# Performance work log

Measured on AMD Instinct MI355X. Metric: run time of the kernel, lower is better.

Reference implementation:

```python
import jax, jax.numpy as jnp
import numpy as np

NUM_HEADS = 16
NUM_KV_HEADS = 4
ROPE_BASE = 10000.0
TRAIN_SEQ_LEN = 2048


def _rms_norm(x):
    eps = jnp.asarray(jnp.finfo(x.dtype).eps, x.dtype)
    return x * jax.lax.rsqrt(jnp.mean(x * x, axis=-1, keepdims=True) + eps)


def _rope_cos_sin(seq_len, head_dim, dtype):
    # seq_len <= TRAIN_SEQ_LEN -> no NTK rescaling, matches Rotary buffer path
    half = head_dim // 2
    inv_freq = 1.0 / (ROPE_BASE ** (jnp.arange(0, head_dim, 2, dtype=jnp.float32) / head_dim))
    t = jnp.arange(seq_len, dtype=jnp.float32)
    freqs = jnp.outer(t, inv_freq)  # [S, half]
    cos = jnp.cos(freqs)[None, :, None, :].astype(dtype)
    sin = jnp.sin(freqs)[None, :, None, :].astype(dtype)
    return cos, sin


def _apply_rotary(x, cos, sin):
    half = x.shape[-1] // 2
    x1, x2 = x[..., :half], x[..., half:]
    return jnp.concatenate([x1 * cos + x2 * sin, -x1 * sin + x2 * cos], axis=-1)


def setup_inputs() -> dict:
    key = jax.random.key(0)
    ks = jax.random.split(key, 5)
    B, S, D = 2, 2048, 2048
    kv_dim = NUM_KV_HEADS * (D // NUM_HEADS)
    sw = 0.02
    return {
        "x": jax.random.normal(ks[0], (B, S, D), jnp.float32),
        "Wq": jax.random.normal(ks[1], (D, D), jnp.float32) * sw,
        "Wk": jax.random.normal(ks[2], (kv_dim, D), jnp.float32) * sw,
        "Wv": jax.random.normal(ks[3], (kv_dim, D), jnp.float32) * sw,
        "Wproj": jax.random.normal(ks[4], (D, D), jnp.float32) * sw,
        "q_gain": jnp.ones((NUM_HEADS,), jnp.float32),
    }


def reference(x, Wq, Wk, Wv, Wproj, q_gain):
    B, S, D = x.shape
    H, Hkv = NUM_HEADS, NUM_KV_HEADS
    hd = D // H
    r = H // Hkv

    q = (x @ Wq.T).reshape(B, S, H, hd)
    k = (x @ Wk.T).reshape(B, S, Hkv, hd)
    v = (x @ Wv.T).reshape(B, S, Hkv, hd)

    q = _rms_norm(q)
    k = _rms_norm(k)

    cos, sin = _rope_cos_sin(S, hd, q.dtype)
    q = _apply_rotary(q, cos, sin)
    k = _apply_rotary(k, cos, sin)
    q = q * q_gain.astype(q.dtype)[None, None, :, None]

    # GQA: repeat kv heads (repeat_interleave along head dim)
    k = jnp.repeat(k, r, axis=2)  # [B,S,H,hd]
    v = jnp.repeat(v, r, axis=2)

    scale = 1.0 / jnp.sqrt(jnp.asarray(hd, q.dtype))
    scores = jnp.einsum("bqhd,bkhd->bhqk", q, k) * scale
    causal = jnp.tril(jnp.ones((S, S), dtype=bool))
    scores = jnp.where(causal[None, None], scores, jnp.asarray(-jnp.inf, scores.dtype))
    attn = jax.nn.softmax(scores, axis=-1)
    y = jnp.einsum("bhqk,bkhd->bqhd", attn, v)

    return y.reshape(B, S, D) @ Wproj.T
```

## Files before the change

kernel.cpp:

```cpp
#include <hip/hip_runtime.h>

#define D_MODEL 2048
#define SEQ 2048
#define BATCH 2
#define NH 16
#define NKV 4
#define HD 128
#define KVD (NKV * HD)
#define QKVN (D_MODEL + 2 * KVD)
#define MROWS (BATCH * SEQ)

typedef __attribute__((ext_vector_type(8))) short short8;
typedef __attribute__((ext_vector_type(4))) float f32x4;

__device__ __forceinline__ unsigned short f2bf(float f) {
    union { float f; unsigned int u; } v; v.f = f;
    unsigned int r = (v.u + 0x7FFFu + ((v.u >> 16) & 1u)) >> 16;
    return (unsigned short)r;
}

__device__ __forceinline__ unsigned short f2bf_pos(float f) {
    union { float f; unsigned int u; } v; v.f = f;
    return (unsigned short)((v.u + 0x8000u) >> 16);
}

__device__ __forceinline__ float bf2f(unsigned short u) {
    union { float f; unsigned int i; } v; v.i = ((unsigned int)u) << 16;
    return v.f;
}

__device__ __forceinline__ void async16(const void* g, void* l) {
    __builtin_amdgcn_global_load_lds((const __attribute__((address_space(1))) void*)g,
                                     (__attribute__((address_space(3))) void*)l, 16, 0, 0);
}

__global__ __launch_bounds__(256) void cast_all(const float* __restrict__ x,
                                                const float* __restrict__ wq,
                                                const float* __restrict__ wk,
                                                const float* __restrict__ wv,
                                                const float* __restrict__ wp,
                                                unsigned short* __restrict__ xb,
                                                unsigned short* __restrict__ wqkv,
                                                unsigned short* __restrict__ wpb) {
    int i = blockIdx.x * 256 + threadIdx.x;
    const float4* s; ushort4* d; int j;
    if (i < 2097152)      { s = (const float4*)x;  d = (ushort4*)xb;             j = i; }
    else if (i < 3145728) { s = (const float4*)wq; d = (ushort4*)wqkv;           j = i - 2097152; }
    else if (i < 3407872) { s = (const float4*)wk; d = (ushort4*)wqkv + 1048576; j = i - 3145728; }
    else if (i < 3670016) { s = (const float4*)wv; d = (ushort4*)wqkv + 1310720; j = i - 3407872; }
    else                  { s = (const float4*)wp; d = (ushort4*)wpb;            j = i - 3670016; }
    float4 v = s[j];
    ushort4 o;
    o.x = f2bf(v.x); o.y = f2bf(v.y); o.z = f2bf(v.z); o.w = f2bf(v.w);
    d[j] = o;
}

__global__ __launch_bounds__(256) void gemm_qkv(const unsigned short* __restrict__ A,
                                                const unsigned short* __restrict__ W,
                                                const float* __restrict__ gain,
                                                unsigned short* __restrict__ qbuf,
                                                unsigned short* __restrict__ kbuf,
                                                unsigned short* __restrict__ vtb) {
    __shared__ unsigned short smem[128 * 137];
    unsigned short* tile = smem;
    const int K = D_MODEL;
    const int tid  = threadIdx.x;
    const int lane = tid & 63;
    const int wave = tid >> 6;
    const int qm   = lane & 15;
    const int quad = lane >> 4;
    const int m0 = blockIdx.y * 128;
    const int bx = blockIdx.x;
    const int n0 = bx * 128;
    const int wm = (wave >> 1) * 64;
    const int wn = (wave & 1) * 64;

    f32x4 acc[4][4];
#pragma unroll
    for (int i = 0; i < 4; i++)
#pragma unroll
        for (int j = 0; j < 4; j++) acc[i][j] = (f32x4){0.f, 0.f, 0.f, 0.f};

    const int r1 = tid >> 2;
    const int c1 = (((tid & 3) ^ ((tid >> 3) & 3)) * 8);
    const unsigned short* Ag = A + (size_t)(m0 + r1) * K + c1;
    const unsigned short* Wg = W + (size_t)(n0 + r1) * K + c1;
    const int stg = wave * 512;
    const int swq = ((qm >> 1) & 3) * 8;

#define STG_Q(bufv) \
    async16(Ag,                  &smem[(bufv) * 4096 + stg]); \
    async16(Ag + (size_t)64 * K, &smem[(bufv) * 4096 + 2048 + stg]); \
    async16(Wg,                  &smem[8192 + (bufv) * 4096 + stg]); \
    async16(Wg + (size_t)64 * K, &smem[8192 + (bufv) * 4096 + 2048 + stg]); \
    Ag += 32; Wg += 32;

#define CMP_Q(bufv) { \
    short8 af[4], bfr[4]; \
    _Pragma("unroll") \
    for (int i = 0; i < 4; i++) { \
        af[i]  = *(const short8*)&smem[(bufv) * 4096 + (wm + i * 16 + qm) * 32 + (quad * 8 ^ swq)]; \
        bfr[i] = *(const short8*)&smem[8192 + (bufv) * 4096 + (wn + i * 16 + qm) * 32 + (quad * 8 ^ swq)]; \
    } \
    __builtin_amdgcn_s_setprio(1); \
    _Pragma("unroll") \
    for (int mi = 0; mi < 4; mi++) \
        _Pragma("unroll") \
        for (int ni = 0; ni < 4; ni++) \
            acc[mi][ni] = __builtin_amdgcn_mfma_f32_16x16x32_bf16(af[mi], bfr[ni], acc[mi][ni], 0, 0, 0); \
    __builtin_amdgcn_s_setprio(0); \
}

    STG_Q(0)
    for (int t = 0; t < 31; ++t) {
        STG_Q(1)
        asm volatile("s_waitcnt vmcnt(4)\n\ts_barrier" ::: "memory");
        CMP_Q(0)
        asm volatile("s_barrier" ::: "memory");
        STG_Q(0)
        asm volatile("s_waitcnt vmcnt(4)\n\ts_barrier" ::: "memory");
        CMP_Q(1)
        asm volatile("s_barrier" ::: "memory");
    }
    STG_Q(1)
    asm volatile("s_waitcnt vmcnt(4)\n\ts_barrier" ::: "memory");
    CMP_Q(0)
    asm volatile("s_waitcnt vmcnt(0)\n\ts_barrier" ::: "memory");
    CMP_Q(1)
    __syncthreads();
#undef STG_Q
#undef CMP_Q

#pragma unroll
    for (int mi = 0; mi < 4; mi++)
#pragma unroll
        for (int r = 0; r < 4; r++) {
            int row = wm + mi * 16 + quad * 4 + r;
#pragma unroll
            for (int ni = 0; ni < 4; ni++)
                tile[row * 137 + wn + ni * 16 + qm] = f2bf(acc[mi][ni][r]);
        }
    __syncthreads();

    const int s_base = m0 & 2047;
    const int bb = m0 >> 11;
    if (bx < 20) {
        const bool isq = bx < 16;
        const float g = isq ? gain[bx] * 0.12751744f : 1.0f;
        unsigned short* dst = isq
            ? qbuf + ((size_t)(bb * NH + bx) * SEQ + s_base) * HD
            : kbuf + ((size_t)(bb * NKV + (bx - 16)) * SEQ + s_base) * HD;
        const float invf = __builtin_amdgcn_exp2f(-(float)lane * 0.20761871f - 2.6514961f);
        for (int rr = 0; rr < 32; rr++) {
            int row = wave * 32 + rr;
            float x1 = bf2f(tile[row * 137 + lane]);
            float x2 = bf2f(tile[row * 137 + 64 + lane]);
            float ss = x1 * x1 + x2 * x2;
            ss += __shfl_xor(ss, 1);  ss += __shfl_xor(ss, 2);  ss += __shfl_xor(ss, 4);
            ss += __shfl_xor(ss, 8);  ss += __shfl_xor(ss, 16); ss += __shfl_xor(ss, 32);
            float rs = rsqrtf(ss * (1.0f / 128.0f) + 1.1920929e-07f);
            float rev = (float)(s_base + row) * invf;
            rev -= truncf(rev);
            float sn = __builtin_amdgcn_sinf(rev);
            float cs = __builtin_amdgcn_cosf(rev);
            float a1 = x1 * rs, a2 = x2 * rs;
            float o1 = (a1 * cs + a2 * sn) * g;
            float o2 = (a2 * cs - a1 * sn) * g;
            dst[(size_t)row * HD + lane]      = f2bf(o1);
            dst[(size_t)row * HD + 64 + lane] = f2bf(o2);
        }
    } else {
        const int hk = bx - 20;
        unsigned short* dst = vtb + ((size_t)(bb * NKV + hk) * HD) * SEQ + s_base;
        const int sc = (tid & 31) * 4;
        const int d0 = tid >> 5;
#pragma unroll
        for (int i = 0; i < 16; i++) {
            int d = d0 + 8 * i;
            ushort4 ov;
            ov.x = tile[(sc + 0) * 137 + d];
            ov.y = tile[(sc + 1) * 137 + d];
            ov.z = tile[(sc + 2) * 137 + d];
            ov.w = tile[(sc + 3) * 137 + d];
            *(ushort4*)(dst + (size_t)d * SEQ + sc) = ov;
        }
    }
}

__global__ __launch_bounds__(256) void gemm_bt(const unsigned short* __restrict__ A,
                                               const unsigned short* __restrict__ W,
                                               float* __restrict__ C, int M, int N, int K) {
    __shared__ unsigned short smem[16384];
    const int tid  = threadIdx.x;
    const int lane = tid & 63;
    const int wave = tid >> 6;
    const int qm   = lane & 15;
    const int quad = lane >> 4;
    const int m0 = blockIdx.y * 128;
    const int n0 = blockIdx.x * 128;
    const int wm = (wave >> 1) * 64;
    const int wn = (wave & 1) * 64;

    f32x4 acc[4][4];
#pragma unroll
    for (int i = 0; i < 4; i++)
#pragma unroll
        for (int j = 0; j < 4; j++) acc[i][j] = (f32x4){0.f, 0.f, 0.f, 0.f};

    const int r1 = tid >> 2;
    const int c1 = (((tid & 3) ^ ((tid >> 3) & 3)) * 8);
    const unsigned short* Ag = A + (size_t)(m0 + r1) * K + c1;
    const unsigned short* Wg = W + (size_t)(n0 + r1) * K + c1;
    const int stg = wave * 512;
    const int swq = ((qm >> 1) & 3) * 8;

#define STG_B(bufv) \
    async16(Ag,                  &smem[(bufv) * 4096 + stg]); \
    async16(Ag + (size_t)64 * K, &smem[(bufv) * 4096 + 2048 + stg]); \
    async16(Wg,                  &smem[8192 + (bufv) * 4096 + stg]); \
    async16(Wg + (size_t)64 * K, &smem[8192 + (bufv) * 4096 + 2048 + stg]); \
    Ag += 32; Wg += 32;

#define CMP_B(bufv) { \
    short8 af[4], bfr[4]; \
    _Pragma("unroll") \
    for (int i = 0; i < 4; i++) { \
        af[i]  = *(const short8*)&smem[(bufv) * 4096 + (wm + i * 16 + qm) * 32 + (quad * 8 ^ swq)]; \
        bfr[i] = *(const short8*)&smem[8192 + (bufv) * 4096 + (wn + i * 16 + qm) * 32 + (quad * 8 ^ swq)]; \
    } \
    __builtin_amdgcn_s_setprio(1); \
    _Pragma("unroll") \
    for (int mi = 0; mi < 4; mi++) \
        _Pragma("unroll") \
        for (int ni = 0; ni < 4; ni++) \
            acc[mi][ni] = __builtin_amdgcn_mfma_f32_16x16x32_bf16(af[mi], bfr[ni], acc[mi][ni], 0, 0, 0); \
    __builtin_amdgcn_s_setprio(0); \
}

    STG_B(0)
    for (int t = 0; t < 31; ++t) {
        STG_B(1)
        asm volatile("s_waitcnt vmcnt(4)\n\ts_barrier" ::: "memory");
        CMP_B(0)
        asm volatile("s_barrier" ::: "memory");
        STG_B(0)
        asm volatile("s_waitcnt vmcnt(4)\n\ts_barrier" ::: "memory");
        CMP_B(1)
        asm volatile("s_barrier" ::: "memory");
    }
    STG_B(1)
    asm volatile("s_waitcnt vmcnt(4)\n\ts_barrier" ::: "memory");
    CMP_B(0)
    asm volatile("s_waitcnt vmcnt(0)\n\ts_barrier" ::: "memory");
    CMP_B(1)
#undef STG_B
#undef CMP_B

#pragma unroll
    for (int mi = 0; mi < 4; mi++) {
#pragma unroll
        for (int r = 0; r < 4; r++) {
            int row = m0 + wm + mi * 16 + quad * 4 + r;
            float* Crow = C + (size_t)row * N + n0 + wn + qm;
#pragma unroll
            for (int ni = 0; ni < 4; ni++) Crow[ni * 16] = acc[mi][ni][r];
        }
    }
}

__global__ __launch_bounds__(256, 4) void attn(const unsigned short* __restrict__ qb,
                                               const unsigned short* __restrict__ kb,
                                               const unsigned short* __restrict__ vt,
                                               const float* __restrict__ gain,
                                               unsigned short* __restrict__ y) {
    __shared__ unsigned short Ks[8192];
    __shared__ unsigned short Vs[8192];
    __shared__ unsigned short plds[4][1024];
    const int tid  = threadIdx.x;
    const int lane = tid & 63;
    const int wave = tid >> 6;
    const int bh   = blockIdx.x & 31;
    const int g4   = blockIdx.x >> 5;
    const int gg = g4 & 7;
    const int gs = g4 >> 3;
    const int qt64 = (gs == 0) ? gg : (gs == 1) ? (31 - gg) : (gs == 2) ? (8 + gg) : (23 - gg);
    const int h = bh & 15;
    const int b = bh >> 4;
    const int qm   = lane & 15;
    const int quad = lane >> 4;
    const int q0    = qt64 * 64;
    const int qrow0 = q0 + wave * 16;
    const float M = 17.0f * fabsf(gain[h]);

    const unsigned short* Qp = qb + (((size_t)(b * NH + h)) * SEQ + qrow0) * HD;
    const unsigned short* Kp = kb + ((size_t)(b * NKV + (h >> 2))) * SEQ * HD;
    const unsigned short* Vp = vt + ((size_t)(b * NKV + (h >> 2))) * HD * SEQ;

    short8 qf[4];
#pragma unroll
    for (int c = 0; c < 4; c++)
        qf[c] = *(const short8*)(Qp + qm * HD + c * 32 + quad * 8);

    f32x4 o[8];
#pragma unroll
    for (int t = 0; t < 8; t++) o[t] = (f32x4){0.f, 0.f, 0.f, 0.f};
    float lr[4] = {0.f, 0.f, 0.f, 0.f};

    const unsigned short* KsA = Kp + (size_t)(tid >> 4) * HD + (((tid & 15) ^ (tid >> 4)) & 15) * 8;
    const unsigned short* VsA = Vp + (size_t)(tid >> 3) * SEQ + (((tid & 7) ^ ((tid >> 3) & 7)) * 8);
    char* KsB = (char*)Ks + wave * 1024;
    char* VsB = (char*)Vs + wave * 1024;
    unsigned short* P = &plds[wave][0];

    const int kvend = q0 + 64;
    for (int kv0 = 0; kv0 < kvend; kv0 += 64) {
#pragma unroll
        for (int i = 0; i < 4; i++) {
            async16(KsA + (size_t)(16 * i) * HD,  KsB + i * 4096);
            async16(VsA + (size_t)(32 * i) * SEQ, VsB + i * 4096);
        }
        KsA += (size_t)64 * HD;
        VsA += 64;
        __syncthreads();

        f32x4 s[4];
#pragma unroll
        for (int g = 0; g < 4; g++) s[g] = (f32x4){0.f, 0.f, 0.f, 0.f};
#pragma unroll
        for (int c = 0; c < 4; c++) {
#pragma unroll
            for (int g = 0; g < 4; g++) {
                short8 kf = *(const short8*)&Ks[(g * 16 + qm) * 128 + (((c * 4 + quad) ^ qm) * 8)];
                s[g] = __builtin_amdgcn_mfma_f32_16x16x32_bf16(qf[c], kf, s[g], 0, 0, 0);
            }
        }
        if (kv0 + 63 > qrow0) {
#pragma unroll
            for (int g = 0; g < 4; g++)
#pragma unroll
                for (int r = 0; r < 4; r++) {
                    int qg = qrow0 + quad * 4 + r;
                    if (kv0 + g * 16 + qm > qg) s[g][r] = -3.0e38f;
                }
        }
        float p[4][4];
#pragma unroll
        for (int g = 0; g < 4; g++)
#pragma unroll
            for (int r = 0; r < 4; r++) {
                p[g][r] = __builtin_amdgcn_exp2f(s[g][r] - M);
                lr[r] += p[g][r];
            }
#pragma unroll
        for (int g = 0; g < 4; g++)
#pragma unroll
            for (int r = 0; r < 4; r++) {
                int rowp = quad * 4 + r;
                P[rowp * 64 + (((g * 2 + (qm >> 3)) ^ (rowp & 7)) * 8) + (qm & 7)] = f2bf_pos(p[g][r]);
            }
        short8 pa[2];
#pragma unroll
        for (int ka = 0; ka < 2; ka++)
            pa[ka] = *(const short8*)&P[qm * 64 + (((ka * 4 + quad) ^ (qm & 7)) * 8)];
#pragma unroll
        for (int t = 0; t < 8; t++) {
#pragma unroll
            for (int ka = 0; ka < 2; ka++) {
                short8 vf = *(const short8*)&Vs[(t * 16 + qm) * 64 + (((ka * 4 + quad) ^ (qm & 7)) * 8)];
                o[t] = __builtin_amdgcn_mfma_f32_16x16x32_bf16(pa[ka], vf, o[t], 0, 0, 0);
            }
        }
        __syncthreads();
    }
    float rl[4];
#pragma unroll
    for (int r = 0; r < 4; r++) {
        float l = lr[r];
        l += __shfl_xor(l, 1);
        l += __shfl_xor(l, 2);
        l += __shfl_xor(l, 4);
        l += __shfl_xor(l, 8);
        rl[r] = 1.0f / l;
    }
#pragma unroll
    for (int t = 0; t < 8; t++) {
#pragma unroll
        for (int r = 0; r < 4; r++) {
            size_t row = (size_t)(b * SEQ + qrow0 + quad * 4 + r);
            y[row * D_MODEL + h * HD + t * 16 + qm] = f2bf(o[t][r] * rl[r]);
        }
    }
}

extern "C" void kernel_launch(void* const* d_in, const int* in_sizes, int n_in,
                              void* d_out, int out_size, void* d_ws, size_t ws_size,
                              hipStream_t stream) {
    const float* x  = (const float*)d_in[0];
    const float* Wq = (const float*)d_in[1];
    const float* Wk = (const float*)d_in[2];
    const float* Wv = (const float*)d_in[3];
    const float* Wp = (const float*)d_in[4];
    const float* qg = (const float*)d_in[5];

    char* ws = (char*)d_ws;
    unsigned short* xb   = (unsigned short*)(ws + 0);
    unsigned short* wqkv = (unsigned short*)(ws + 16777216);
    unsigned short* wp   = (unsigned short*)(ws + 29360128);
    unsigned short* qbuf = (unsigned short*)(ws + 37748736);
    unsigned short* kbuf = (unsigned short*)(ws + 54525952);
    unsigned short* vtb  = (unsigned short*)(ws + 58720256);
    unsigned short* y    = xb;

    cast_all<<<18432, 256, 0, stream>>>(x, Wq, Wk, Wv, Wp, xb, wqkv, wp);
    gemm_qkv<<<dim3(24, 32), 256, 0, stream>>>(xb, wqkv, qg, qbuf, kbuf, vtb);
    attn<<<1024, 256, 0, stream>>>(qbuf, kbuf, vtb, qg, y);
    gemm_bt<<<dim3(16, 32), 256, 0, stream>>>(y, wp, (float*)d_out, MROWS, D_MODEL, D_MODEL);
}
```

Baseline: 292.2 us.

## Enlarge QKV GEMM to 256x256 tiles with 8 waves and ping-pong pipeline

The fused QKV projection GEMM moves from 128x128 tiles with 4 waves to 256x256 tiles with 8 waves and 512 threads per block. Each K step is now 64 wide and staged in quarter-tile pieces that interleave with MFMA groups, with double-buffered LDS. The epilogue (RMSNorm, RoPE and the V transpose) is done in two halves that reuse the LDS. The intent is more operand reuse per byte loaded and better overlap of loads with MFMA, at the cost of a much smaller grid (192 blocks on a chip with more CUs) and 128KB of LDS per block, which limits occupancy.

```diff
diff --git a/kernel.cpp b/kernel.cpp
--- a/kernel.cpp
+++ b/kernel.cpp
@@ -55,13 +55,13 @@
     d[j] = o;
 }
 
-__global__ __launch_bounds__(256) void gemm_qkv(const unsigned short* __restrict__ A,
+__global__ __launch_bounds__(512) void gemm_qkv(const unsigned short* __restrict__ A,
                                                 const unsigned short* __restrict__ W,
                                                 const float* __restrict__ gain,
                                                 unsigned short* __restrict__ qbuf,
                                                 unsigned short* __restrict__ kbuf,
                                                 unsigned short* __restrict__ vtb) {
-    __shared__ unsigned short smem[128 * 137];
+    __shared__ unsigned short smem[65536];
     unsigned short* tile = smem;
     const int K = D_MODEL;
     const int tid  = threadIdx.x;
@@ -69,120 +69,169 @@
     const int wave = tid >> 6;
     const int qm   = lane & 15;
     const int quad = lane >> 4;
-    const int m0 = blockIdx.y * 128;
+    const int wr   = wave >> 2;
+    const int wc   = wave & 3;
+    const int m0 = blockIdx.y * 256;
     const int bx = blockIdx.x;
-    const int n0 = bx * 128;
-    const int wm = (wave >> 1) * 64;
-    const int wn = (wave & 1) * 64;
-
-    f32x4 acc[4][4];
-#pragma unroll
-    for (int i = 0; i < 4; i++)
-#pragma unroll
-        for (int j = 0; j < 4; j++) acc[i][j] = (f32x4){0.f, 0.f, 0.f, 0.f};
-
-    const int r1 = tid >> 2;
-    const int c1 = (((tid & 3) ^ ((tid >> 3) & 3)) * 8);
-    const unsigned short* Ag = A + (size_t)(m0 + r1) * K + c1;
-    const unsigned short* Wg = W + (size_t)(n0 + r1) * K + c1;
-    const int stg = wave * 512;
-    const int swq = ((qm >> 1) & 3) * 8;
-
-#define STG_Q(bufv) \
-    async16(Ag,                  &smem[(bufv) * 4096 + stg]); \
-    async16(Ag + (size_t)64 * K, &smem[(bufv) * 4096 + 2048 + stg]); \
-    async16(Wg,                  &smem[8192 + (bufv) * 4096 + stg]); \
-    async16(Wg + (size_t)64 * K, &smem[8192 + (bufv) * 4096 + 2048 + stg]); \
-    Ag += 32; Wg += 32;
-
-#define CMP_Q(bufv) { \
-    short8 af[4], bfr[4]; \
+    const int n0 = bx * 256;
+
+    f32x4 acc[2][2][4][2];
+#pragma unroll
+    for (int a = 0; a < 2; a++)
+#pragma unroll
+        for (int b = 0; b < 2; b++)
+#pragma unroll
+            for (int c = 0; c < 4; c++)
+#pragma unroll
+                for (int d = 0; d < 2; d++) acc[a][b][c][d] = (f32x4){0.f, 0.f, 0.f, 0.f};
+
+    const unsigned short* Asrc = A + (size_t)(m0 + (tid >> 3)) * K + (((tid & 7) ^ ((tid >> 3) & 7)) * 8);
+    const unsigned short* Bsrc = W + (size_t)(n0 + (tid >> 3)) * K + (((tid & 7) ^ ((tid >> 3) & 7)) * 8);
+    const int dstg = tid * 8;
+    const int ck0 = ((quad ^ (qm & 7)) * 8);
+    const int ck1 = (((4 + quad) ^ (qm & 7)) * 8);
+    const int arow = wr * 64 + qm;
+    const int brow = wc * 32 + qm;
+
+    short8 af[4][2], bf0[2][2], bf1[2][2];
+
+#define STG_A(mh, bufv, kt1) \
+    async16(Asrc + (size_t)((mh) * 128) * K + (kt1),      &smem[(bufv) * 16384 + (mh) * 8192 + dstg]); \
+    async16(Asrc + (size_t)((mh) * 128 + 64) * K + (kt1), &smem[(bufv) * 16384 + (mh) * 8192 + 4096 + dstg]);
+#define STG_B(nh, bufv, kt1) \
+    async16(Bsrc + (size_t)((nh) * 128) * K + (kt1),      &smem[32768 + (bufv) * 16384 + (nh) * 8192 + dstg]); \
+    async16(Bsrc + (size_t)((nh) * 128 + 64) * K + (kt1), &smem[32768 + (bufv) * 16384 + (nh) * 8192 + 4096 + dstg]);
+
+#define RD_A(ab, mh) { \
     _Pragma("unroll") \
-    for (int i = 0; i < 4; i++) { \
-        af[i]  = *(const short8*)&smem[(bufv) * 4096 + (wm + i * 16 + qm) * 32 + (quad * 8 ^ swq)]; \
-        bfr[i] = *(const short8*)&smem[8192 + (bufv) * 4096 + (wn + i * 16 + qm) * 32 + (quad * 8 ^ swq)]; \
-    } \
+    for (int m = 0; m < 4; m++) { \
+        af[m][0] = *(const short8*)&smem[(ab) + ((mh) * 128 + arow + m * 16) * 64 + ck0]; \
+        af[m][1] = *(const short8*)&smem[(ab) + ((mh) * 128 + arow + m * 16) * 64 + ck1]; \
+    } }
+#define RD_B(bb, nh, dstf) { \
+    _Pragma("unroll") \
+    for (int n = 0; n < 2; n++) { \
+        dstf[n][0] = *(const short8*)&smem[(bb) + ((nh) * 128 + brow + n * 16) * 64 + ck0]; \
+        dstf[n][1] = *(const short8*)&smem[(bb) + ((nh) * 128 + brow + n * 16) * 64 + ck1]; \
+    } }
+#define MFMA16(mh, nh, bfr) { \
     __builtin_amdgcn_s_setprio(1); \
     _Pragma("unroll") \
-    for (int mi = 0; mi < 4; mi++) \
+    for (int m = 0; m < 4; m++) \
         _Pragma("unroll") \
-        for (int ni = 0; ni < 4; ni++) \
-            acc[mi][ni] = __builtin_amdgcn_mfma_f32_16x16x32_bf16(af[mi], bfr[ni], acc[mi][ni], 0, 0, 0); \
-    __builtin_amdgcn_s_setprio(0); \
-}
-
-    STG_Q(0)
-    for (int t = 0; t < 31; ++t) {
-        STG_Q(1)
-        asm volatile("s_waitcnt vmcnt(4)\n\ts_barrier" ::: "memory");
-        CMP_Q(0)
-        asm volatile("s_barrier" ::: "memory");
-        STG_Q(0)
-        asm volatile("s_waitcnt vmcnt(4)\n\ts_barrier" ::: "memory");
-        CMP_Q(1)
-        asm volatile("s_barrier" ::: "memory");
-    }
-    STG_Q(1)
-    asm volatile("s_waitcnt vmcnt(4)\n\ts_barrier" ::: "memory");
-    CMP_Q(0)
-    asm volatile("s_waitcnt vmcnt(0)\n\ts_barrier" ::: "memory");
-    CMP_Q(1)
-    __syncthreads();
-#undef STG_Q
-#undef CMP_Q
-
-#pragma unroll
-    for (int mi = 0; mi < 4; mi++)
-#pragma unroll
-        for (int r = 0; r < 4; r++) {
-            int row = wm + mi * 16 + quad * 4 + r;
-#pragma unroll
-            for (int ni = 0; ni < 4; ni++)
-                tile[row * 137 + wn + ni * 16 + qm] = f2bf(acc[mi][ni][r]);
-        }
-    __syncthreads();
+        for (int n = 0; n < 2; n++) { \
+            acc[mh][nh][m][n] = __builtin_amdgcn_mfma_f32_16x16x32_bf16(af[m][0], bfr[n][0], acc[mh][nh][m][n], 0, 0, 0); \
+            acc[mh][nh][m][n] = __builtin_amdgcn_mfma_f32_16x16x32_bf16(af[m][1], bfr[n][1], acc[mh][nh][m][n], 0, 0, 0); \
+        } \
+    __builtin_amdgcn_s_setprio(0); }
+
+#define BARv asm volatile("s_barrier" ::: "memory")
+#define WV4  asm volatile("s_waitcnt vmcnt(4)" ::: "memory")
+#define WV2  asm volatile("s_waitcnt vmcnt(2)" ::: "memory")
+#define WV0  asm volatile("s_waitcnt vmcnt(0)" ::: "memory")
+
+#define STEP(p, kt1) { \
+     RD_A((p)*16384, 0) RD_B(32768 + (p)*16384, 0, bf0) STG_A(0, (p)^1, kt1) \
+    BARv; MFMA16(0, 0, bf0) WV4; BARv; \
+     RD_B(32768 + (p)*16384, 1, bf1) STG_B(0, (p)^1, kt1) \
+    BARv; MFMA16(0, 1, bf1) WV4; BARv; \
+     RD_A((p)*16384, 1) STG_B(1, (p)^1, kt1) \
+    BARv; MFMA16(1, 0, bf0) BARv; \
+     STG_A(1, (p)^1, kt1) \
+    BARv; MFMA16(1, 1, bf1) WV4; BARv; \
+}
+#define STEPE(p) { \
+    RD_A((p)*16384, 0) RD_B(32768 + (p)*16384, 0, bf0) BARv; MFMA16(0, 0, bf0) WV2; BARv; \
+    RD_B(32768 + (p)*16384, 1, bf1)                    BARv; MFMA16(0, 1, bf1) WV0; BARv; \
+    RD_A((p)*16384, 1)                                 BARv; MFMA16(1, 0, bf0) BARv; \
+    MFMA16(1, 1, bf1) \
+}
+
+    STG_A(0, 0, 0) STG_B(0, 0, 0) STG_B(1, 0, 0) STG_A(1, 0, 0)
+    WV4; BARv;
+
+#pragma unroll 1
+    for (int t2 = 0; t2 < 15; ++t2) {
+        STEP(0, t2 * 128 + 64)
+        STEP(1, t2 * 128 + 128)
+    }
+    STEP(0, 1984)
+    STEPE(1)
+#undef STG_A
+#undef STG_B
+#undef RD_A
+#undef RD_B
+#undef MFMA16
+#undef STEP
+#undef STEPE
 
     const int s_base = m0 & 2047;
     const int bb = m0 >> 11;
-    if (bx < 20) {
-        const bool isq = bx < 16;
-        const float g = isq ? gain[bx] * 0.12751744f : 1.0f;
-        unsigned short* dst = isq
-            ? qbuf + ((size_t)(bb * NH + bx) * SEQ + s_base) * HD
-            : kbuf + ((size_t)(bb * NKV + (bx - 16)) * SEQ + s_base) * HD;
-        const float invf = __builtin_amdgcn_exp2f(-(float)lane * 0.20761871f - 2.6514961f);
-        for (int rr = 0; rr < 32; rr++) {
-            int row = wave * 32 + rr;
-            float x1 = bf2f(tile[row * 137 + lane]);
-            float x2 = bf2f(tile[row * 137 + 64 + lane]);
-            float ss = x1 * x1 + x2 * x2;
-            ss += __shfl_xor(ss, 1);  ss += __shfl_xor(ss, 2);  ss += __shfl_xor(ss, 4);
-            ss += __shfl_xor(ss, 8);  ss += __shfl_xor(ss, 16); ss += __shfl_xor(ss, 32);
-            float rs = rsqrtf(ss * (1.0f / 128.0f) + 1.1920929e-07f);
-            float rev = (float)(s_base + row) * invf;
-            rev -= truncf(rev);
-            float sn = __builtin_amdgcn_sinf(rev);
-            float cs = __builtin_amdgcn_cosf(rev);
-            float a1 = x1 * rs, a2 = x2 * rs;
-            float o1 = (a1 * cs + a2 * sn) * g;
-            float o2 = (a2 * cs - a1 * sn) * g;
-            dst[(size_t)row * HD + lane]      = f2bf(o1);
-            dst[(size_t)row * HD + 64 + lane] = f2bf(o2);
-        }
-    } else {
-        const int hk = bx - 20;
-        unsigned short* dst = vtb + ((size_t)(bb * NKV + hk) * HD) * SEQ + s_base;
-        const int sc = (tid & 31) * 4;
-        const int d0 = tid >> 5;
-#pragma unroll
-        for (int i = 0; i < 16; i++) {
-            int d = d0 + 8 * i;
-            ushort4 ov;
-            ov.x = tile[(sc + 0) * 137 + d];
-            ov.y = tile[(sc + 1) * 137 + d];
-            ov.z = tile[(sc + 2) * 137 + d];
-            ov.w = tile[(sc + 3) * 137 + d];
-            *(ushort4*)(dst + (size_t)d * SEQ + sc) = ov;
+    const float invf = __builtin_amdgcn_exp2f(-(float)lane * 0.20761871f - 2.6514961f);
+
+#pragma unroll
+    for (int half = 0; half < 2; ++half) {
+        __syncthreads();
+#pragma unroll
+        for (int nh = 0; nh < 2; nh++)
+#pragma unroll
+            for (int m = 0; m < 4; m++)
+#pragma unroll
+                for (int n = 0; n < 2; n++)
+#pragma unroll
+                    for (int r = 0; r < 4; r++) {
+                        int row = wr * 64 + m * 16 + quad * 4 + r;
+                        int col = nh * 128 + wc * 32 + n * 16 + qm;
+                        tile[row * 264 + col] = f2bf(acc[half][nh][m][n][r]);
+                    }
+        __syncthreads();
+
+        if (bx < 10) {
+            const bool isq = bx < 8;
+#pragma unroll
+            for (int hh = 0; hh < 2; hh++) {
+                const int h = (isq ? 2 * bx : (bx - 8) * 2) + hh;
+                const float g = isq ? gain[h] * 0.12751744f : 1.0f;
+                unsigned short* dst = isq
+                    ? qbuf + ((size_t)(bb * NH + h) * SEQ + s_base + half * 128) * HD
+                    : kbuf + ((size_t)(bb * NKV + h) * SEQ + s_base + half * 128) * HD;
+                for (int rr = 0; rr < 16; rr++) {
+                    int row = wave * 16 + rr;
+                    float x1 = bf2f(tile[row * 264 + hh * 128 + lane]);
+                    float x2 = bf2f(tile[row * 264 + hh * 128 + 64 + lane]);
+                    float ss = x1 * x1 + x2 * x2;
+                    ss += __shfl_xor(ss, 1);  ss += __shfl_xor(ss, 2);  ss += __shfl_xor(ss, 4);
+                    ss += __shfl_xor(ss, 8);  ss += __shfl_xor(ss, 16); ss += __shfl_xor(ss, 32);
+                    float rs = rsqrtf(ss * (1.0f / 128.0f) + 1.1920929e-07f);
+                    float rev = (float)(s_base + half * 128 + row) * invf;
+                    rev -= truncf(rev);
+                    float sn = __builtin_amdgcn_sinf(rev);
+                    float cs = __builtin_amdgcn_cosf(rev);
+                    float a1 = x1 * rs, a2 = x2 * rs;
+                    float o1 = (a1 * cs + a2 * sn) * g;
+                    float o2 = (a2 * cs - a1 * sn) * g;
+                    dst[(size_t)row * HD + lane]      = f2bf(o1);
+                    dst[(size_t)row * HD + 64 + lane] = f2bf(o2);
+                }
+            }
+        } else {
+            const int sc = (tid & 31) * 4;
+            const int d0 = tid >> 5;
+#pragma unroll
+            for (int hh = 0; hh < 2; hh++) {
+                const int hk = (bx - 10) * 2 + hh;
+                unsigned short* dstv = vtb + ((size_t)(bb * NKV + hk) * HD) * SEQ + s_base + half * 128;
+#pragma unroll
+                for (int i = 0; i < 8; i++) {
+                    int d = d0 + 16 * i;
+                    ushort4 ov;
+                    ov.x = tile[(sc + 0) * 264 + hh * 128 + d];
+                    ov.y = tile[(sc + 1) * 264 + hh * 128 + d];
+                    ov.z = tile[(sc + 2) * 264 + hh * 128 + d];
+                    ov.w = tile[(sc + 3) * 264 + hh * 128 + d];
+                    *(ushort4*)(dstv + (size_t)d * SEQ + sc) = ov;
+                }
+            }
         }
     }
 }
@@ -412,7 +461,7 @@
     unsigned short* y    = xb;
 
     cast_all<<<18432, 256, 0, stream>>>(x, Wq, Wk, Wv, Wp, xb, wqkv, wp);
-    gemm_qkv<<<dim3(24, 32), 256, 0, stream>>>(xb, wqkv, qg, qbuf, kbuf, vtb);
+    gemm_qkv<<<dim3(12, 16), 512, 0, stream>>>(xb, wqkv, qg, qbuf, kbuf, vtb);
     attn<<<1024, 256, 0, stream>>>(qbuf, kbuf, vtb, qg, y);
     gemm_bt<<<dim3(16, 32), 256, 0, stream>>>(y, wp, (float*)d_out, MROWS, D_MODEL, D_MODEL);
 }
```

After: 285.8 us. -2.2%, faster.
